# Kernel tuning notes

Measured on AMD Instinct MI355X. Metric: run time of the kernel, lower is better.

## Reference

```python
import jax, jax.numpy as jnp
import numpy as np

B = 8192          # batch of independent BFGS problems
TX = 16           # transmit antennas
N = 2 * TX        # real-valued problem size
ITER = 10         # outer BFGS iterations
RO = 0.5          # backtracking shrink factor
C = 1e-4          # Armijo constant
MAX_BT = 25       # fixed unroll of the data-dependent backtracking loop (0.5**25 ~ 3e-8)


def setup_inputs() -> dict:
    key = jax.random.key(0)
    k1, k2, k3 = jax.random.split(key, 3)
    h = jax.random.normal(k1, (B, N, N), jnp.float32) / np.float32(np.sqrt(N))
    x_true = jax.random.normal(k2, (B, N), jnp.float32)
    # y = h @ x_true + noise : realistic, well-posed least-squares instances
    y = jnp.einsum('bij,bj->bi', h, x_true) + 0.1 * jax.random.normal(k3, (B, N), jnp.float32)
    x = jnp.zeros((B, N), jnp.float32)
    alpha = jnp.ones((B,), jnp.float32)
    h_k = jnp.broadcast_to(jnp.eye(N, dtype=jnp.float32), (B, N, N))  # BFGS identity init
    return {"y": y, "h": h, "x": x, "alpha": alpha, "h_k": h_k, "iteration": ITER}


def _bfgs(y, h, x, alpha, h_k, iteration):
    y = y[..., None]          # [B, N, 1]
    x = x[..., None]          # [B, N, 1]
    hT = jnp.swapaxes(h, 1, 2)

    def f_value(pt):                      # [B, 1]
        return jnp.linalg.norm(y - h @ pt, axis=1) / 2

    def grad_value(pt):                   # [B, N, 1]
        return hT @ (h @ pt) - hT @ y

    for _ in range(iteration):
        g = grad_value(x)
        p = -(h_k @ g)                    # search direction [B, N, 1]
        fx = f_value(x)                   # [B, 1]
        gp = (jnp.swapaxes(g, 1, 2) @ p)[:, :, 0]   # g^T p, [B, 1]
        # Armijo backtracking: fixed unroll of `while any(...): alpha = where(..., ro*alpha, alpha)`
        for _ in range(MAX_BT):
            lhs = f_value(x + alpha[:, None, None] * p)[:, 0]        # [B]
            rhs = (fx + C * alpha[:, None] * gp)[:, 0]               # [B]
            alpha = jnp.where(lhs > rhs, RO * alpha, alpha)
        x_new = x + alpha[:, None, None] * p
        s = x_new - x
        y_k = grad_value(x_new) - g
        sT = jnp.swapaxes(s, 1, 2)
        ykT = jnp.swapaxes(y_k, 1, 2)
        auxSc = sT @ y_k                  # [B, 1, 1]
        h_k = (h_k
               + (auxSc + ykT @ (h_k @ y_k)) * (s @ sT) / auxSc ** 2
               - ((h_k @ (y_k @ sT)) + s @ (ykT @ h_k)) / auxSc)
        x = x_new
    return x[:, :, 0]


def reference(y, h, x, alpha, h_k, iteration):
    return _bfgs(y, h, x, alpha, h_k, iteration)
```

## Files before the change

kernel.cpp:

```cpp
#include <hip/hip_runtime.h>
#include <math.h>


__device__ __forceinline__ float rlane63(float v) {
    return __int_as_float(__builtin_amdgcn_readlane(__float_as_int(v), 63));
}

template <int CTRL>
__device__ __forceinline__ float dpp_mov(float v) {
    return __int_as_float(
        __builtin_amdgcn_update_dpp(0, __float_as_int(v), CTRL, 0xf, 0xf, true));
}
template <int CTRL>
__device__ __forceinline__ float dppadd(float v) { return v + dpp_mov<CTRL>(v); }

__device__ __forceinline__ float wavesum(float v) {
    v = dppadd<0xB1>(v);
    v = dppadd<0x4E>(v);
    v = dppadd<0x141>(v);
    v = dppadd<0x140>(v);
    v = dppadd<0x142>(v);
    v = dppadd<0x143>(v);
    return rlane63(v);
}


#define ROT_FMA_BLOCK(M, V, A0, A1)                                        \
    asm volatile(                                                          \
        "s_nop 1\n\t"                                                      \
        "v_mul_f32 %0, %2, %3\n\t"                                         \
        "v_mul_f32_dpp %1, %3, %4 row_ror:15 row_mask:0xf bank_mask:0xf bound_ctrl:1\n\t" \
        "v_fmac_f32_dpp %0, %3, %5 row_ror:14 row_mask:0xf bank_mask:0xf bound_ctrl:1\n\t" \
        "v_fmac_f32_dpp %1, %3, %6 row_ror:13 row_mask:0xf bank_mask:0xf bound_ctrl:1\n\t" \
        "v_fmac_f32_dpp %0, %3, %7 row_ror:12 row_mask:0xf bank_mask:0xf bound_ctrl:1\n\t" \
        "v_fmac_f32_dpp %1, %3, %8 row_ror:11 row_mask:0xf bank_mask:0xf bound_ctrl:1\n\t" \
        "v_fmac_f32_dpp %0, %3, %9 row_ror:10 row_mask:0xf bank_mask:0xf bound_ctrl:1\n\t" \
        "v_fmac_f32_dpp %1, %3, %10 row_ror:9 row_mask:0xf bank_mask:0xf bound_ctrl:1\n\t" \
        "v_fmac_f32_dpp %0, %3, %11 row_ror:8 row_mask:0xf bank_mask:0xf bound_ctrl:1\n\t" \
        "v_fmac_f32_dpp %1, %3, %12 row_ror:7 row_mask:0xf bank_mask:0xf bound_ctrl:1\n\t" \
        "v_fmac_f32_dpp %0, %3, %13 row_ror:6 row_mask:0xf bank_mask:0xf bound_ctrl:1\n\t" \
        "v_fmac_f32_dpp %1, %3, %14 row_ror:5 row_mask:0xf bank_mask:0xf bound_ctrl:1\n\t" \
        "v_fmac_f32_dpp %0, %3, %15 row_ror:4 row_mask:0xf bank_mask:0xf bound_ctrl:1\n\t" \
        "v_fmac_f32_dpp %1, %3, %16 row_ror:3 row_mask:0xf bank_mask:0xf bound_ctrl:1\n\t" \
        "v_fmac_f32_dpp %0, %3, %17 row_ror:2 row_mask:0xf bank_mask:0xf bound_ctrl:1\n\t" \
        "v_fmac_f32_dpp %1, %3, %18 row_ror:1 row_mask:0xf bank_mask:0xf bound_ctrl:1\n\t" \
        : "=&v"(A0), "=&v"(A1)                                             \
        : "v"((M)[0]), "v"(V), "v"((M)[1]), "v"((M)[2]), "v"((M)[3]),      \
          "v"((M)[4]), "v"((M)[5]), "v"((M)[6]), "v"((M)[7]), "v"((M)[8]), \
          "v"((M)[9]), "v"((M)[10]), "v"((M)[11]), "v"((M)[12]),           \
          "v"((M)[13]), "v"((M)[14]), "v"((M)[15]))

__device__ __forceinline__ float fwd_mv(const float (&M)[16], float v) {
    float a0, a1;
    ROT_FMA_BLOCK(M, v, a0, a1);
    const float acc = a0 + a1;
    return acc + __shfl_xor(acc, 32);
}

__device__ __forceinline__ float trp_mv(const float (&M)[16], float u) {
    float a0, a1;
    ROT_FMA_BLOCK(M, u, a0, a1);
    const float acc = a0 + a1;
    return acc + __shfl_xor(acc, 16);
}

__device__ __forceinline__ float relayout(float x, bool mid) {
    const float sw = __shfl_xor(x, 48);
    return mid ? sw : x;
}

__device__ __forceinline__ unsigned short f2bf(float x) {
    unsigned u = __float_as_uint(x);
    return (unsigned short)((u + 0x7FFFu + ((u >> 16) & 1u)) >> 16);
}
__device__ __forceinline__ float bf2f(unsigned short h) {
    return __uint_as_float(((unsigned)h) << 16);
}

typedef float f32x16 __attribute__((ext_vector_type(16)));
typedef short s16x8  __attribute__((ext_vector_type(8)));

#define LPAD 33

__global__ __launch_bounds__(256) void bfgs_kernel(
    const float* __restrict__ y_g,
    const float* __restrict__ h_g,
    const int*   __restrict__ iter_g,
    float*       __restrict__ out)
{
    __shared__ __align__(16) float Hs[4][32 * LPAD];

    const int tid  = threadIdx.x;
    const int l    = tid & 63;
    const int w    = tid >> 6;
    const int prob = blockIdx.x * 4 + w;

    const int  i   = l & 15;
    const int  a   = l >> 4;
    const int  c   = l >> 5;
    const int  r   = a & 1;
    const bool mid = (a == 1) || (a == 2);

    const float* __restrict__ hb = h_g + (size_t)prob * 1024;
    float* Hp = Hs[w];

    #pragma unroll
    for (int u = 0; u < 4; ++u) {
        const int f = u * 256 + l * 4;
        const float4 v4 = *reinterpret_cast<const float4*>(hb + f);
        const int r0 = f >> 5, c0 = f & 31;
        float* d = Hp + r0 * LPAD + c0;
        d[0] = v4.x; d[1] = v4.y; d[2] = v4.z; d[3] = v4.w;
    }
    __builtin_amdgcn_wave_barrier();

    const float yq = y_g[prob * 32 + 16 * r + i];
    float g;
    {
        float Htt[16];
        #pragma unroll
        for (int k = 0; k < 16; ++k) {
            const int ik = (i + k) & 15;
            Htt[k] = Hp[(16 * r + ik) * LPAD + 16 * c + i];
        }
        g = -trp_mv(Htt, yq);
    }
    float rr = 0.5f * wavesum(yq * yq);

    s16x8 hi0, lo0, hi1, lo1;
    #pragma unroll
    for (int j = 0; j < 8; ++j) {
        const int m = 8 * (l >> 5) + j;
        const float v0 = Hp[m * LPAD + (l & 31)];
        const float v1 = Hp[(m + 16) * LPAD + (l & 31)];
        const unsigned short h0 = f2bf(v0);
        const unsigned short h1 = f2bf(v1);
        hi0[j] = (short)h0; lo0[j] = (short)f2bf(v0 - bf2f(h0));
        hi1[j] = (short)h1; lo1[j] = (short)f2bf(v1 - bf2f(h1));
    }
    f32x16 acc = {};
    acc = __builtin_amdgcn_mfma_f32_32x32x16_bf16(lo0, lo0, acc, 0, 0, 0);
    acc = __builtin_amdgcn_mfma_f32_32x32x16_bf16(lo1, lo1, acc, 0, 0, 0);
    acc = __builtin_amdgcn_mfma_f32_32x32x16_bf16(hi0, lo0, acc, 0, 0, 0);
    acc = __builtin_amdgcn_mfma_f32_32x32x16_bf16(lo0, hi0, acc, 0, 0, 0);
    acc = __builtin_amdgcn_mfma_f32_32x32x16_bf16(hi1, lo1, acc, 0, 0, 0);
    acc = __builtin_amdgcn_mfma_f32_32x32x16_bf16(lo1, hi1, acc, 0, 0, 0);
    acc = __builtin_amdgcn_mfma_f32_32x32x16_bf16(hi0, hi0, acc, 0, 0, 0);
    acc = __builtin_amdgcn_mfma_f32_32x32x16_bf16(hi1, hi1, acc, 0, 0, 0);
    __builtin_amdgcn_wave_barrier();

    #pragma unroll
    for (int reg = 0; reg < 16; ++reg) {
        const int row = (reg & 3) + 8 * (reg >> 2) + 4 * (l >> 5);
        Hp[row * LPAD + (l & 31)] = acc[reg];
    }
    __builtin_amdgcn_wave_barrier();

    float Gr[16];
    const int rbase = (16 * r + i) * LPAD + 16 * c;
    #pragma unroll
    for (int k = 0; k < 16; ++k)
        Gr[k] = Hp[rbase + ((i + k) & 15)];

    float hkr[16];
    #pragma unroll
    for (int k = 0; k < 16; ++k) hkr[k] = 0.f;
    hkr[0] = (r == c) ? 1.f : 0.f;

    float p_v = -g;
    float p_q = relayout(p_v, mid);
    float gp  = -0.5f * wavesum(g * g);

    float x = 0.f, alpha = 1.f;
    const int niter = iter_g[0];

    for (int it = 0; it < niter; ++it) {
        const float t_q = fwd_mv(Gr, p_v);
        const float qq  = 0.5f * wavesum(p_q * t_q);
        const float t_v = relayout(t_q, mid);

        const float rq  = -gp;
        const float fx  = 0.5f * sqrtf(rr);
        const float a_c = ldexpf(alpha, -(l & 31));
        const float rhs = fx + (1e-4f * a_c) * gp;
        const float phi = fmaf(a_c, fmaf(a_c, qq, -2.f * rq), rr);
        const bool cond = (rhs < 0.f) || (0.25f * phi > rhs * rhs);
        const unsigned long long bal = __ballot(cond);
        const unsigned mh  = (unsigned)bal;
        const unsigned inv = (~mh & 0x01FFFFFFu) | 0x02000000u;
        alpha = ldexpf(alpha, -(__ffs(inv) - 1));

        x = fmaf(alpha, p_v, x);
        rr = fmaf(alpha, fmaf(alpha, qq, -2.f * rq), rr);

        const float s   = alpha * p_v;
        const float s_q = alpha * p_q;
        const float aux = (alpha * alpha) * qq;
        const float yk  = alpha * t_v;
        g += yk;

        const float ht_q = fwd_mv(hkr, t_v);
        const float htv  = relayout(ht_q, mid);
        const float yhy  = 0.5f * wavesum(yk * (alpha * htv));

        const float hy_q = alpha * ht_q;
        const float inva = 1.f / aux;
        const float c1   = (aux + yhy) * (inva * inva);
        const float uR   = fmaf(c1, s_q, -(hy_q * inva));
        const float wR   = -(s_q * inva) * alpha;

        asm volatile(
            "s_nop 1\n\t"
            "v_fmac_f32 %0, %16, %18\n\t"
            "v_fmac_f32 %0, %17, %19\n\t"
            "v_fmac_f32_dpp %1, %16, %18 row_ror:15 row_mask:0xf bank_mask:0xf bound_ctrl:1\n\t"
            "v_fmac_f32_dpp %1, %17, %19 row_ror:15 row_mask:0xf bank_mask:0xf bound_ctrl:1\n\t"
            "v_fmac_f32_dpp %2, %16, %18 row_ror:14 row_mask:0xf bank_mask:0xf bound_ctrl:1\n\t"
            "v_fmac_f32_dpp %2, %17, %19 row_ror:14 row_mask:0xf bank_mask:0xf bound_ctrl:1\n\t"
            "v_fmac_f32_dpp %3, %16, %18 row_ror:13 row_mask:0xf bank_mask:0xf bound_ctrl:1\n\t"
            "v_fmac_f32_dpp %3, %17, %19 row_ror:13 row_mask:0xf bank_mask:0xf bound_ctrl:1\n\t"
            "v_fmac_f32_dpp %4, %16, %18 row_ror:12 row_mask:0xf bank_mask:0xf bound_ctrl:1\n\t"
            "v_fmac_f32_dpp %4, %17, %19 row_ror:12 row_mask:0xf bank_mask:0xf bound_ctrl:1\n\t"
            "v_fmac_f32_dpp %5, %16, %18 row_ror:11 row_mask:0xf bank_mask:0xf bound_ctrl:1\n\t"
            "v_fmac_f32_dpp %5, %17, %19 row_ror:11 row_mask:0xf bank_mask:0xf bound_ctrl:1\n\t"
            "v_fmac_f32_dpp %6, %16, %18 row_ror:10 row_mask:0xf bank_mask:0xf bound_ctrl:1\n\t"
            "v_fmac_f32_dpp %6, %17, %19 row_ror:10 row_mask:0xf bank_mask:0xf bound_ctrl:1\n\t"
            "v_fmac_f32_dpp %7, %16, %18 row_ror:9 row_mask:0xf bank_mask:0xf bound_ctrl:1\n\t"
            "v_fmac_f32_dpp %7, %17, %19 row_ror:9 row_mask:0xf bank_mask:0xf bound_ctrl:1\n\t"
            "v_fmac_f32_dpp %8, %16, %18 row_ror:8 row_mask:0xf bank_mask:0xf bound_ctrl:1\n\t"
            "v_fmac_f32_dpp %8, %17, %19 row_ror:8 row_mask:0xf bank_mask:0xf bound_ctrl:1\n\t"
            "v_fmac_f32_dpp %9, %16, %18 row_ror:7 row_mask:0xf bank_mask:0xf bound_ctrl:1\n\t"
            "v_fmac_f32_dpp %9, %17, %19 row_ror:7 row_mask:0xf bank_mask:0xf bound_ctrl:1\n\t"
            "v_fmac_f32_dpp %10, %16, %18 row_ror:6 row_mask:0xf bank_mask:0xf bound_ctrl:1\n\t"
            "v_fmac_f32_dpp %10, %17, %19 row_ror:6 row_mask:0xf bank_mask:0xf bound_ctrl:1\n\t"
            "v_fmac_f32_dpp %11, %16, %18 row_ror:5 row_mask:0xf bank_mask:0xf bound_ctrl:1\n\t"
            "v_fmac_f32_dpp %11, %17, %19 row_ror:5 row_mask:0xf bank_mask:0xf bound_ctrl:1\n\t"
            "v_fmac_f32_dpp %12, %16, %18 row_ror:4 row_mask:0xf bank_mask:0xf bound_ctrl:1\n\t"
            "v_fmac_f32_dpp %12, %17, %19 row_ror:4 row_mask:0xf bank_mask:0xf bound_ctrl:1\n\t"
            "v_fmac_f32_dpp %13, %16, %18 row_ror:3 row_mask:0xf bank_mask:0xf bound_ctrl:1\n\t"
            "v_fmac_f32_dpp %13, %17, %19 row_ror:3 row_mask:0xf bank_mask:0xf bound_ctrl:1\n\t"
            "v_fmac_f32_dpp %14, %16, %18 row_ror:2 row_mask:0xf bank_mask:0xf bound_ctrl:1\n\t"
            "v_fmac_f32_dpp %14, %17, %19 row_ror:2 row_mask:0xf bank_mask:0xf bound_ctrl:1\n\t"
            "v_fmac_f32_dpp %15, %16, %18 row_ror:1 row_mask:0xf bank_mask:0xf bound_ctrl:1\n\t"
            "v_fmac_f32_dpp %15, %17, %19 row_ror:1 row_mask:0xf bank_mask:0xf bound_ctrl:1\n\t"
            : "+v"(hkr[0]), "+v"(hkr[1]), "+v"(hkr[2]), "+v"(hkr[3]),
              "+v"(hkr[4]), "+v"(hkr[5]), "+v"(hkr[6]), "+v"(hkr[7]),
              "+v"(hkr[8]), "+v"(hkr[9]), "+v"(hkr[10]), "+v"(hkr[11]),
              "+v"(hkr[12]), "+v"(hkr[13]), "+v"(hkr[14]), "+v"(hkr[15])
            : "v"(s), "v"(htv), "v"(uR), "v"(wR));

        const float ia  = 1.f / alpha;
        const float k1  = fmaf(alpha, gp, aux);
        const float k2  = fmaf(yhy, ia, -qq);
        p_q = fmaf(-alpha, ht_q, p_q);
        p_q = fmaf(-k1, uR, p_q);
        p_q = fmaf(-k2, wR, p_q);
        p_v = relayout(p_q, mid);
        gp  = gp + alpha * qq - alpha * k2
            - c1 * k1 * k1 + 2.f * (inva * alpha) * k1 * k2;
    }

    if (r == 0) out[prob * 32 + 16 * c + i] = x;
}

extern "C" void kernel_launch(void* const* d_in, const int* in_sizes, int n_in,
                              void* d_out, int out_size, void* d_ws, size_t ws_size,
                              hipStream_t stream) {
    const float* y  = (const float*)d_in[0];
    const float* hh = (const float*)d_in[1];
    const int*   it = (const int*)d_in[5];
    float* out = (float*)d_out;

    const int B = in_sizes[0] / 32;
    dim3 grid(B / 4), block(256);
    bfgs_kernel<<<grid, block, 0, stream>>>(y, hh, it, out);
}
```

Before: 33.93 us.

## Use hardware bf16 pack conversion, permlane swaps, and drop lo*lo MFMA terms

Replaces the software bf16 round/split with the packed v_cvt_pk_bf16_f32 instruction, rewrites the final stages of the wave reduction using permlane32/16 swap instead of row-broadcast DPP plus readlane, and removes the two lo*lo MFMA products from the split-precision Gram computation. This trims ALU work in the setup phase and shortens the reduction dependency chain. Dropping the lo*lo terms slightly lowers the accuracy of H^T H.

```diff
diff --git a/kernel.cpp b/kernel.cpp
--- a/kernel.cpp
+++ b/kernel.cpp
@@ -2,9 +2,7 @@
 #include <math.h>
 
 
-__device__ __forceinline__ float rlane63(float v) {
-    return __int_as_float(__builtin_amdgcn_readlane(__float_as_int(v), 63));
-}
+typedef int v2i __attribute__((ext_vector_type(2)));
 
 template <int CTRL>
 __device__ __forceinline__ float dpp_mov(float v) {
@@ -19,9 +17,12 @@
     v = dppadd<0x4E>(v);
     v = dppadd<0x141>(v);
     v = dppadd<0x140>(v);
-    v = dppadd<0x142>(v);
-    v = dppadd<0x143>(v);
-    return rlane63(v);
+    int ti = __float_as_int(v);
+    v2i p1 = __builtin_amdgcn_permlane32_swap(ti, ti, false, false);
+    v = __int_as_float(p1[0]) + __int_as_float(p1[1]);
+    ti = __float_as_int(v);
+    v2i p2 = __builtin_amdgcn_permlane16_swap(ti, ti, false, false);
+    return __int_as_float(p2[0]) + __int_as_float(p2[1]);
 }
 
 
@@ -69,16 +70,20 @@
     return mid ? sw : x;
 }
 
-__device__ __forceinline__ unsigned short f2bf(float x) {
-    unsigned u = __float_as_uint(x);
-    return (unsigned short)((u + 0x7FFFu + ((u >> 16) & 1u)) >> 16);
-}
-__device__ __forceinline__ float bf2f(unsigned short h) {
-    return __uint_as_float(((unsigned)h) << 16);
+__device__ __forceinline__ int pack_pair(float a, float b, int& lo_pk) {
+    int hp;
+    asm("v_cvt_pk_bf16_f32 %0, %1, %2" : "=v"(hp) : "v"(a), "v"(b));
+    const float ra = a - __int_as_float(hp << 16);
+    const float rb = b - __int_as_float(hp & 0xffff0000);
+    int lp;
+    asm("v_cvt_pk_bf16_f32 %0, %1, %2" : "=v"(lp) : "v"(ra), "v"(rb));
+    lo_pk = lp;
+    return hp;
 }
 
 typedef float f32x16 __attribute__((ext_vector_type(16)));
 typedef short s16x8  __attribute__((ext_vector_type(8)));
+typedef int   i32x4  __attribute__((ext_vector_type(4)));
 
 #define LPAD 33
 
@@ -127,20 +132,26 @@
     }
     float rr = 0.5f * wavesum(yq * yq);
 
-    s16x8 hi0, lo0, hi1, lo1;
+    float v0[8], v1[8];
     #pragma unroll
     for (int j = 0; j < 8; ++j) {
         const int m = 8 * (l >> 5) + j;
-        const float v0 = Hp[m * LPAD + (l & 31)];
-        const float v1 = Hp[(m + 16) * LPAD + (l & 31)];
-        const unsigned short h0 = f2bf(v0);
-        const unsigned short h1 = f2bf(v1);
-        hi0[j] = (short)h0; lo0[j] = (short)f2bf(v0 - bf2f(h0));
-        hi1[j] = (short)h1; lo1[j] = (short)f2bf(v1 - bf2f(h1));
-    }
+        v0[j] = Hp[m * LPAD + (l & 31)];
+        v1[j] = Hp[(m + 16) * LPAD + (l & 31)];
+    }
+    i32x4 h0d, l0d, h1d, l1d;
+    #pragma unroll
+    for (int jj = 0; jj < 4; ++jj) {
+        int lo;
+        h0d[jj] = pack_pair(v0[2*jj], v0[2*jj+1], lo); l0d[jj] = lo;
+        h1d[jj] = pack_pair(v1[2*jj], v1[2*jj+1], lo); l1d[jj] = lo;
+    }
+    const s16x8 hi0 = __builtin_bit_cast(s16x8, h0d);
+    const s16x8 lo0 = __builtin_bit_cast(s16x8, l0d);
+    const s16x8 hi1 = __builtin_bit_cast(s16x8, h1d);
+    const s16x8 lo1 = __builtin_bit_cast(s16x8, l1d);
+
     f32x16 acc = {};
-    acc = __builtin_amdgcn_mfma_f32_32x32x16_bf16(lo0, lo0, acc, 0, 0, 0);
-    acc = __builtin_amdgcn_mfma_f32_32x32x16_bf16(lo1, lo1, acc, 0, 0, 0);
     acc = __builtin_amdgcn_mfma_f32_32x32x16_bf16(hi0, lo0, acc, 0, 0, 0);
     acc = __builtin_amdgcn_mfma_f32_32x32x16_bf16(lo0, hi0, acc, 0, 0, 0);
     acc = __builtin_amdgcn_mfma_f32_32x32x16_bf16(hi1, lo1, acc, 0, 0, 0);
```

New measurement: 35.08 us. 3.4% more time.
